# Performance work log

Measured on AMD Instinct MI355X. Metric: run time of the kernel, lower is better.

The kernel has to match this reference:

```python
import jax, jax.numpy as jnp
import numpy as np

B, N, IN_F, OUT_F, H = 16, 1024, 256, 256, 4
D = OUT_F // H  # head_dim = 64
NEG_SLOPE = 0.2


def setup_inputs() -> dict:
    key = jax.random.key(0)
    k1, k2, k3 = jax.random.split(key, 3)
    h = jax.random.normal(k1, (B, N, IN_F), dtype=jnp.float32)
    mask = jnp.ones((B, N), dtype=jnp.int32)
    W = jax.random.normal(k2, (OUT_F, IN_F), dtype=jnp.float32) * (1.0 / np.sqrt(IN_F))
    a = jax.random.normal(k3, (2 * D, 1), dtype=jnp.float32) * 0.1
    return {"h": h, "mask": mask, "W": W, "a": a}


def reference(h, mask, W, a):
    # Wh = h @ W.T -> (B, N, OUT_F) -> (B, H, N, D)
    Wh = jnp.einsum('bnf,of->bno', h, W)
    Wh = Wh.reshape(h.shape[0], h.shape[1], H, D).transpose(0, 2, 1, 3)
    # Additive split: cat([Wh_i, Wh_j]) @ a == Wh_i @ a1 + Wh_j @ a2 (same math,
    # avoids the O(N^2 * 2D) concat tensor)
    a1 = a[:D, 0]  # (D,)
    a2 = a[D:, 0]  # (D,)
    s1 = jnp.einsum('bhnd,d->bhn', Wh, a1)  # score for node i
    s2 = jnp.einsum('bhnd,d->bhn', Wh, a2)  # score for node j
    e = s1[:, :, :, None] + s2[:, :, None, :]          # (B, H, N, N)
    e = jnp.where(e >= 0, e, NEG_SLOPE * e)            # LeakyReLU(0.2)
    node_mask = mask.astype(bool)                      # (B, N)
    mm = node_mask[:, None, :, None] & node_mask[:, None, None, :]  # (B,1,N,N)
    e = jnp.where(mm, e, -jnp.inf)
    attn = jax.nn.softmax(e, axis=-1)
    # dropout is identity in eval mode
    attn = jnp.where(mm, attn, 0.0)
    h_prime = jnp.einsum('bhij,bhjd->bhid', attn, Wh)  # (B, H, N, D)
    h_prime = h_prime.transpose(0, 2, 1, 3).reshape(h.shape[0], h.shape[1], OUT_F)
    return h_prime * mask.astype(h_prime.dtype)[:, :, None]
```

## Files before the change

### kernel.cpp

```cpp
#include <hip/hip_runtime.h>

typedef short short8 __attribute__((ext_vector_type(8)));
typedef float floatx4 __attribute__((ext_vector_type(4)));
typedef float floatx16 __attribute__((ext_vector_type(16)));
typedef unsigned int u32;

#define NEG_SLOPE 0.2f

__device__ __forceinline__ u32 pk_rtne(float a, float b) {
    u32 ua = __float_as_uint(a); ua += 0x7fffu + ((ua >> 16) & 1u);
    u32 ub = __float_as_uint(b); ub += 0x7fffu + ((ub >> 16) & 1u);
    return __builtin_amdgcn_perm(ub, ua, 0x07060302);
}
__device__ __forceinline__ u32 pk_trunc(float a, float b) {
    return __builtin_amdgcn_perm(__float_as_uint(b), __float_as_uint(a), 0x07060302);
}
__device__ __forceinline__ void gl_lds16(const void* g, void* l) {
    __builtin_amdgcn_global_load_lds((__attribute__((address_space(1))) u32*)(void*)g,
                                     (__attribute__((address_space(3))) u32*)l, 16, 0, 0);
}

__global__ __launch_bounds__(256, 4) void k_prep(
    const float* __restrict__ W, const float* __restrict__ a,
    unsigned short* __restrict__ WFg, float* __restrict__ V1g,
    float* __restrict__ V2g)
{
    __shared__ float sV1[256], sV2[256];
    const int t = threadIdx.x;
    const int hh = blockIdx.x;
    const int lane = t & 63;

    sV1[t] = 0.f;
    sV2[t] = 0.f;
    __syncthreads();

    float vp1[8] = {0, 0, 0, 0, 0, 0, 0, 0};
    float vp2[8] = {0, 0, 0, 0, 0, 0, 0, 0};
    const int c = t & 31;
    const int rb = t >> 5;
#pragma unroll
    for (int i = 0; i < 8; ++i) {
        int row = i * 8 + rb;
        const float* gp = &W[((size_t)(hh * 64 + row)) * 256 + c * 8];
        float4 w0 = *(const float4*)gp;
        float4 w1 = *(const float4*)(gp + 4);
        float a1r = a[row], a2r = a[64 + row];
        vp1[0] += a1r * w0.x; vp1[1] += a1r * w0.y; vp1[2] += a1r * w0.z; vp1[3] += a1r * w0.w;
        vp1[4] += a1r * w1.x; vp1[5] += a1r * w1.y; vp1[6] += a1r * w1.z; vp1[7] += a1r * w1.w;
        vp2[0] += a2r * w0.x; vp2[1] += a2r * w0.y; vp2[2] += a2r * w0.z; vp2[3] += a2r * w0.w;
        vp2[4] += a2r * w1.x; vp2[5] += a2r * w1.y; vp2[6] += a2r * w1.z; vp2[7] += a2r * w1.w;
        uint4 pv;
        pv.x = pk_rtne(w0.x, w0.y); pv.y = pk_rtne(w0.z, w0.w);
        pv.z = pk_rtne(w1.x, w1.y); pv.w = pk_rtne(w1.z, w1.w);
        int kt = c >> 2, qq = c & 3, nt = row >> 4, r15 = row & 15;
        int idx16 = (kt * 4 + nt) * 64 + qq * 16 + r15;
        *(uint4*)&WFg[((size_t)hh * 2048 + idx16) * 8] = pv;
    }
#pragma unroll
    for (int j = 0; j < 8; ++j) {
        vp1[j] += __shfl_xor(vp1[j], 32, 64);
        vp2[j] += __shfl_xor(vp2[j], 32, 64);
    }
    if (lane < 32) {
#pragma unroll
        for (int j = 0; j < 8; ++j) {
            atomicAdd(&sV1[c * 8 + j], vp1[j]);
            atomicAdd(&sV2[c * 8 + j], vp2[j]);
        }
    }
    __syncthreads();
    V1g[hh * 256 + t] = sV1[t];
    V2g[hh * 256 + t] = sV2[t];
}

__global__ __launch_bounds__(256, 4) void k_wh(
    const float* __restrict__ hin, const int* __restrict__ mask,
    const unsigned short* __restrict__ WFg, const float* __restrict__ V1g,
    const float* __restrict__ V2g,
    unsigned short* __restrict__ WhF, float2* __restrict__ E1F1,
    float2* __restrict__ E2F2)
{
    __shared__ unsigned short sBF[8 * 4 * 64 * 8];
    __shared__ float sV1[256], sV2[256];

    const int t = threadIdx.x;
    const int bi = blockIdx.x;
    const int mtile = bi & 255, hh = bi >> 8;
    const int m0g = mtile * 64;
    const int b = m0g >> 10, i0 = m0g & 1023;
    const int b4h = b * 4 + hh;
    const int wid = t >> 6, lane = t & 63;
    const int l15 = lane & 15, q = lane >> 4;

    {
        const char* wsrc = (const char*)WFg + (size_t)hh * 32768;
#pragma unroll
        for (int r = 0; r < 8; ++r)
            gl_lds16(wsrc + r * 4096 + t * 16, (char*)sBF + r * 4096 + t * 16);
        if (wid == 0)
            gl_lds16((const char*)(V1g + hh * 256) + lane * 16, (char*)sV1 + lane * 16);
        if (wid == 1)
            gl_lds16((const char*)(V2g + hh * 256) + lane * 16, (char*)sV2 + lane * 16);
    }
    __syncthreads();

    floatx4 acc[4];
#pragma unroll
    for (int nt = 0; nt < 4; ++nt) {
        floatx4 z = {0.f, 0.f, 0.f, 0.f};
        acc[nt] = z;
    }
    float s1a = 0.f, s2a = 0.f;
    const float* hrow = &hin[((size_t)(m0g + wid * 16 + l15)) * 256 + q * 8];
#pragma unroll
    for (int kt = 0; kt < 8; ++kt) {
        float4 h0 = *(const float4*)(hrow + kt * 32);
        float4 h1 = *(const float4*)(hrow + kt * 32 + 4);
        float4 v1a = *(const float4*)&sV1[kt * 32 + q * 8];
        float4 v1b = *(const float4*)&sV1[kt * 32 + q * 8 + 4];
        float4 v2a = *(const float4*)&sV2[kt * 32 + q * 8];
        float4 v2b = *(const float4*)&sV2[kt * 32 + q * 8 + 4];
        s1a += h0.x * v1a.x + h0.y * v1a.y + h0.z * v1a.z + h0.w * v1a.w
             + h1.x * v1b.x + h1.y * v1b.y + h1.z * v1b.z + h1.w * v1b.w;
        s2a += h0.x * v2a.x + h0.y * v2a.y + h0.z * v2a.z + h0.w * v2a.w
             + h1.x * v2b.x + h1.y * v2b.y + h1.z * v2b.z + h1.w * v2b.w;
        union { short8 s; uint4 u; } af;
        af.u.x = pk_rtne(h0.x, h0.y); af.u.y = pk_rtne(h0.z, h0.w);
        af.u.z = pk_rtne(h1.x, h1.y); af.u.w = pk_rtne(h1.z, h1.w);
#pragma unroll
        for (int nt = 0; nt < 4; ++nt) {
            short8 bf = *(const short8*)&sBF[((kt * 4 + nt) * 64 + lane) * 8];
            acc[nt] = __builtin_amdgcn_mfma_f32_16x16x32_bf16(af.s, bf, acc[nt], 0, 0, 0);
        }
    }

    const int jt16 = (i0 >> 4) + wid;
    const int g = q & 1, jb = (q >> 1) * 4;
#pragma unroll
    for (int nt = 0; nt < 4; ++nt) {
        int nt32 = nt >> 1;
        int l31 = (nt & 1) * 16 + l15;
        uint2 pv;
        pv.x = pk_rtne(acc[nt][0], acc[nt][1]);
        pv.y = pk_rtne(acc[nt][2], acc[nt][3]);
        size_t idx = ((((size_t)b4h * 64 + jt16) * 2 + nt32) * 64 + (g * 32 + l31)) * 8 + jb;
        *(uint2*)&WhF[idx] = pv;
    }

    s1a += __shfl_xor(s1a, 16, 64); s1a += __shfl_xor(s1a, 32, 64);
    s2a += __shfl_xor(s2a, 16, 64); s2a += __shfl_xor(s2a, 32, 64);
    if (lane < 16) {
        int i = i0 + wid * 16 + lane;
        E1F1[(size_t)b4h * 1024 + i] = make_float2(__expf(s1a), __expf(NEG_SLOPE * s1a));
        int mj = mask[b * 1024 + i];
        E2F2[(size_t)b4h * 1024 + i] =
            make_float2(mj ? __expf(s2a) : 0.f, mj ? __expf(NEG_SLOPE * s2a) : 0.f);
    }
}

__global__ __launch_bounds__(256, 4) void k_attn(
    const int* __restrict__ mask,
    const unsigned short* __restrict__ WhF,
    const float2* __restrict__ E1F1, const float2* __restrict__ E2F2,
    float* __restrict__ out)
{
    __shared__ float2 sEF[1024];
    __shared__ float sRed[2][64][49];

    const int t = threadIdx.x;
    const int bi = blockIdx.x;
    const int b4h = bi & 63, ib = bi >> 6;
    const int b = b4h >> 2, hh = b4h & 3;
    const int i0 = ib * 64;
    const int wid = t >> 6, lane = t & 63;
    const int l31 = lane & 31, g = lane >> 5;
    const int rg = wid & 1, jh = wid >> 1;
    const int iw = i0 + rg * 32;

    {
        const char* src = (const char*)(E2F2 + (size_t)b4h * 1024);
        gl_lds16(src + t * 16, (char*)sEF + t * 16);
        gl_lds16(src + 4096 + t * 16, (char*)sEF + 4096 + t * 16);
    }

    float2 e1 = E1F1[(size_t)b4h * 1024 + iw + l31];
    const float E1 = e1.x, F1 = e1.y;

    floatx16 acc0, acc1, accL;
#pragma unroll
    for (int r = 0; r < 16; ++r) { acc0[r] = 0.f; acc1[r] = 0.f; accL[r] = 0.f; }
    const short ob = (short)0x3F80;
    const short8 ones = {ob, ob, ob, ob, ob, ob, ob, ob};

    const char* gbase = (const char*)WhF + (size_t)b4h * 131072 + (size_t)lane * 16;
    const int cb = jh * 32;

    short8 ga0 = *(const short8*)(gbase + (size_t)cb * 2048);
    short8 ga1 = *(const short8*)(gbase + (size_t)cb * 2048 + 1024);
    short8 gb0 = *(const short8*)(gbase + (size_t)(cb + 1) * 2048);
    short8 gb1 = *(const short8*)(gbase + (size_t)(cb + 1) * 2048 + 1024);

    __syncthreads();

    float4 nA0, nA1, nB0, nB1;
    {
        const float4* pA = (const float4*)&sEF[cb * 16 + g * 4];
        const float4* pB = (const float4*)&sEF[cb * 16 + 8 + g * 4];
        nA0 = pA[0]; nA1 = pA[1]; nB0 = pB[0]; nB1 = pB[1];
    }

#pragma unroll 4
    for (int cr = 0; cr < 32; cr += 2) {
        {
            const float4 eA0 = nA0, eA1 = nA1, eB0 = nB0, eB1 = nB1;
            const int cn = cb + ((cr + 1) & 31);
            const float4* pA = (const float4*)&sEF[cn * 16 + g * 4];
            const float4* pB = (const float4*)&sEF[cn * 16 + 8 + g * 4];
            nA0 = pA[0]; nA1 = pA[1]; nB0 = pB[0]; nB1 = pB[1];
            const short8 bf0 = ga0, bf1 = ga1;
            const int cg = cb + ((cr + 2) & 31);
            ga0 = *(const short8*)(gbase + (size_t)cg * 2048);
            ga1 = *(const short8*)(gbase + (size_t)cg * 2048 + 1024);
            float w0 = fmaxf(E1 * eA0.x, F1 * eA0.y);
            float w1 = fmaxf(E1 * eA0.z, F1 * eA0.w);
            float w2 = fmaxf(E1 * eA1.x, F1 * eA1.y);
            float w3 = fmaxf(E1 * eA1.z, F1 * eA1.w);
            float w4 = fmaxf(E1 * eB0.x, F1 * eB0.y);
            float w5 = fmaxf(E1 * eB0.z, F1 * eB0.w);
            float w6 = fmaxf(E1 * eB1.x, F1 * eB1.y);
            float w7 = fmaxf(E1 * eB1.z, F1 * eB1.w);
            union { short8 s; u32 u[4]; } af;
            af.u[0] = pk_trunc(w0, w1);
            af.u[1] = pk_trunc(w2, w3);
            af.u[2] = pk_trunc(w4, w5);
            af.u[3] = pk_trunc(w6, w7);
            acc0 = __builtin_amdgcn_mfma_f32_32x32x16_bf16(af.s, bf0, acc0, 0, 0, 0);
            acc1 = __builtin_amdgcn_mfma_f32_32x32x16_bf16(af.s, bf1, acc1, 0, 0, 0);
            accL = __builtin_amdgcn_mfma_f32_32x32x16_bf16(af.s, ones, accL, 0, 0, 0);
        }
        {
            const float4 eA0 = nA0, eA1 = nA1, eB0 = nB0, eB1 = nB1;
            const int cn = cb + ((cr + 2) & 31);
            const float4* pA = (const float4*)&sEF[cn * 16 + g * 4];
            const float4* pB = (const float4*)&sEF[cn * 16 + 8 + g * 4];
            nA0 = pA[0]; nA1 = pA[1]; nB0 = pB[0]; nB1 = pB[1];
            const short8 bf0 = gb0, bf1 = gb1;
            const int cg = cb + ((cr + 3) & 31);
            gb0 = *(const short8*)(gbase + (size_t)cg * 2048);
            gb1 = *(const short8*)(gbase + (size_t)cg * 2048 + 1024);
            float w0 = fmaxf(E1 * eA0.x, F1 * eA0.y);
            float w1 = fmaxf(E1 * eA0.z, F1 * eA0.w);
            float w2 = fmaxf(E1 * eA1.x, F1 * eA1.y);
            float w3 = fmaxf(E1 * eA1.z, F1 * eA1.w);
            float w4 = fmaxf(E1 * eB0.x, F1 * eB0.y);
            float w5 = fmaxf(E1 * eB0.z, F1 * eB0.w);
            float w6 = fmaxf(E1 * eB1.x, F1 * eB1.y);
            float w7 = fmaxf(E1 * eB1.z, F1 * eB1.w);
            union { short8 s; u32 u[4]; } af;
            af.u[0] = pk_trunc(w0, w1);
            af.u[1] = pk_trunc(w2, w3);
            af.u[2] = pk_trunc(w4, w5);
            af.u[3] = pk_trunc(w6, w7);
            acc0 = __builtin_amdgcn_mfma_f32_32x32x16_bf16(af.s, bf0, acc0, 0, 0, 0);
            acc1 = __builtin_amdgcn_mfma_f32_32x32x16_bf16(af.s, bf1, acc1, 0, 0, 0);
            accL = __builtin_amdgcn_mfma_f32_32x32x16_bf16(af.s, ones, accL, 0, 0, 0);
        }
    }

    if (jh == 1) {
        float* d = &sRed[rg][lane][0];
#pragma unroll
        for (int r = 0; r < 16; ++r) {
            d[r] = acc0[r]; d[16 + r] = acc1[r]; d[32 + r] = accL[r];
        }
    }
    __syncthreads();
    if (jh == 0) {
        const float* d = &sRed[rg][lane][0];
#pragma unroll
        for (int r = 0; r < 16; ++r) {
            acc0[r] += d[r]; acc1[r] += d[16 + r]; accL[r] += d[32 + r];
        }
#pragma unroll
        for (int r = 0; r < 16; ++r) {
            int row = (r & 3) + 8 * (r >> 2) + 4 * g;
            int i = iw + row;
            float l = accL[r];
            int mi = mask[b * 1024 + i];
            float inv = (mi && l > 0.f) ? 1.0f / l : 0.f;
            size_t o = ((size_t)(b * 1024 + i)) * 256 + hh * 64;
            out[o + l31] = acc0[r] * inv;
            out[o + 32 + l31] = acc1[r] * inv;
        }
    }
}

extern "C" void kernel_launch(void* const* d_in, const int* in_sizes, int n_in,
                              void* d_out, int out_size, void* d_ws, size_t ws_size,
                              hipStream_t stream) {
    const float* h = (const float*)d_in[0];
    const int* mask = (const int*)d_in[1];
    const float* W = (const float*)d_in[2];
    const float* a = (const float*)d_in[3];
    float* out = (float*)d_out;

    unsigned short* WhF = (unsigned short*)d_ws;
    float2* E1F1 = (float2*)((char*)d_ws + (size_t)8 * 1024 * 1024);
    float2* E2F2 = E1F1 + 64 * 1024;
    unsigned short* WFg = (unsigned short*)((char*)d_ws + (size_t)9 * 1024 * 1024);
    float* V1g = (float*)((char*)WFg + 4 * 16384 * sizeof(unsigned short));
    float* V2g = V1g + 1024;

    hipLaunchKernelGGL(k_prep, dim3(4), dim3(256), 0, stream, W, a, WFg, V1g, V2g);
    hipLaunchKernelGGL(k_wh, dim3(1024), dim3(256), 0, stream, h, mask, WFg, V1g, V2g, WhF, E1F1, E2F2);
    hipLaunchKernelGGL(k_attn, dim3(1024), dim3(256), 0, stream, mask, WhF, E1F1, E2F2, out);
}
```

Measured before the change: 101.7 us.

## Prepermute E2F2 exponent table and read it from global instead of LDS

k_wh now writes the per-node exp scores in a permuted layout, so each lane's eight needed values for one MFMA k-step are contiguous. k_attn then loads them directly from global memory (cached in L1/L2) as four float4s, dropping the LDS staging buffer, the global-to-LDS copy and the block barrier. This lowers LDS use and removes a sync, but the inner loop now issues extra global loads that may add latency.

```diff
diff --git a/kernel.cpp b/kernel.cpp
--- a/kernel.cpp
+++ b/kernel.cpp
@@ -78,7 +78,7 @@
     const unsigned short* __restrict__ WFg, const float* __restrict__ V1g,
     const float* __restrict__ V2g,
     unsigned short* __restrict__ WhF, float2* __restrict__ E1F1,
-    float2* __restrict__ E2F2)
+    float2* __restrict__ EFp)
 {
     __shared__ unsigned short sBF[8 * 4 * 64 * 8];
     __shared__ float sV1[256], sV2[256];
@@ -153,18 +153,20 @@
         int i = i0 + wid * 16 + lane;
         E1F1[(size_t)b4h * 1024 + i] = make_float2(__expf(s1a), __expf(NEG_SLOPE * s1a));
         int mj = mask[b * 1024 + i];
-        E2F2[(size_t)b4h * 1024 + i] =
-            make_float2(mj ? __expf(s2a) : 0.f, mj ? __expf(NEG_SLOPE * s2a) : 0.f);
+        float e2v = mj ? __expf(s2a) : 0.f;
+        float f2v = mj ? __expf(NEG_SLOPE * s2a) : 0.f;
+        int cc = i >> 4, rr = i & 15;
+        int gg = (rr >> 2) & 1, jj = (rr & 3) + 4 * (rr >> 3);
+        EFp[(size_t)b4h * 1024 + (cc * 2 + gg) * 8 + jj] = make_float2(e2v, f2v);
     }
 }
 
 __global__ __launch_bounds__(256, 4) void k_attn(
     const int* __restrict__ mask,
     const unsigned short* __restrict__ WhF,
-    const float2* __restrict__ E1F1, const float2* __restrict__ E2F2,
+    const float2* __restrict__ E1F1, const float2* __restrict__ EFp,
     float* __restrict__ out)
 {
-    __shared__ float2 sEF[1024];
     __shared__ float sRed[2][64][49];
 
     const int t = threadIdx.x;
@@ -177,12 +179,6 @@
     const int rg = wid & 1, jh = wid >> 1;
     const int iw = i0 + rg * 32;
 
-    {
-        const char* src = (const char*)(E2F2 + (size_t)b4h * 1024);
-        gl_lds16(src + t * 16, (char*)sEF + t * 16);
-        gl_lds16(src + 4096 + t * 16, (char*)sEF + 4096 + t * 16);
-    }
-
     float2 e1 = E1F1[(size_t)b4h * 1024 + iw + l31];
     const float E1 = e1.x, F1 = e1.y;
 
@@ -193,42 +189,38 @@
     const short8 ones = {ob, ob, ob, ob, ob, ob, ob, ob};
 
     const char* gbase = (const char*)WhF + (size_t)b4h * 131072 + (size_t)lane * 16;
+    const float4* efb = (const float4*)(EFp + (size_t)b4h * 1024);
     const int cb = jh * 32;
 
     short8 ga0 = *(const short8*)(gbase + (size_t)cb * 2048);
     short8 ga1 = *(const short8*)(gbase + (size_t)cb * 2048 + 1024);
     short8 gb0 = *(const short8*)(gbase + (size_t)(cb + 1) * 2048);
     short8 gb1 = *(const short8*)(gbase + (size_t)(cb + 1) * 2048 + 1024);
-
-    __syncthreads();
-
-    float4 nA0, nA1, nB0, nB1;
+    float4 nE0, nE1, nE2, nE3;
     {
-        const float4* pA = (const float4*)&sEF[cb * 16 + g * 4];
-        const float4* pB = (const float4*)&sEF[cb * 16 + 8 + g * 4];
-        nA0 = pA[0]; nA1 = pA[1]; nB0 = pB[0]; nB1 = pB[1];
+        const float4* p = efb + (size_t)(cb * 2 + g) * 4;
+        nE0 = p[0]; nE1 = p[1]; nE2 = p[2]; nE3 = p[3];
     }
 
 #pragma unroll 4
     for (int cr = 0; cr < 32; cr += 2) {
         {
-            const float4 eA0 = nA0, eA1 = nA1, eB0 = nB0, eB1 = nB1;
+            const float4 e0 = nE0, e1v = nE1, e2v = nE2, e3v = nE3;
             const int cn = cb + ((cr + 1) & 31);
-            const float4* pA = (const float4*)&sEF[cn * 16 + g * 4];
-            const float4* pB = (const float4*)&sEF[cn * 16 + 8 + g * 4];
-            nA0 = pA[0]; nA1 = pA[1]; nB0 = pB[0]; nB1 = pB[1];
+            const float4* p = efb + (size_t)(cn * 2 + g) * 4;
+            nE0 = p[0]; nE1 = p[1]; nE2 = p[2]; nE3 = p[3];
             const short8 bf0 = ga0, bf1 = ga1;
             const int cg = cb + ((cr + 2) & 31);
             ga0 = *(const short8*)(gbase + (size_t)cg * 2048);
             ga1 = *(const short8*)(gbase + (size_t)cg * 2048 + 1024);
-            float w0 = fmaxf(E1 * eA0.x, F1 * eA0.y);
-            float w1 = fmaxf(E1 * eA0.z, F1 * eA0.w);
-            float w2 = fmaxf(E1 * eA1.x, F1 * eA1.y);
-            float w3 = fmaxf(E1 * eA1.z, F1 * eA1.w);
-            float w4 = fmaxf(E1 * eB0.x, F1 * eB0.y);
-            float w5 = fmaxf(E1 * eB0.z, F1 * eB0.w);
-            float w6 = fmaxf(E1 * eB1.x, F1 * eB1.y);
-            float w7 = fmaxf(E1 * eB1.z, F1 * eB1.w);
+            float w0 = fmaxf(E1 * e0.x, F1 * e0.y);
+            float w1 = fmaxf(E1 * e0.z, F1 * e0.w);
+            float w2 = fmaxf(E1 * e1v.x, F1 * e1v.y);
+            float w3 = fmaxf(E1 * e1v.z, F1 * e1v.w);
+            float w4 = fmaxf(E1 * e2v.x, F1 * e2v.y);
+            float w5 = fmaxf(E1 * e2v.z, F1 * e2v.w);
+            float w6 = fmaxf(E1 * e3v.x, F1 * e3v.y);
+            float w7 = fmaxf(E1 * e3v.z, F1 * e3v.w);
             union { short8 s; u32 u[4]; } af;
             af.u[0] = pk_trunc(w0, w1);
             af.u[1] = pk_trunc(w2, w3);
@@ -239,23 +231,22 @@
             accL = __builtin_amdgcn_mfma_f32_32x32x16_bf16(af.s, ones, accL, 0, 0, 0);
         }
         {
-            const float4 eA0 = nA0, eA1 = nA1, eB0 = nB0, eB1 = nB1;
+            const float4 e0 = nE0, e1v = nE1, e2v = nE2, e3v = nE3;
             const int cn = cb + ((cr + 2) & 31);
-            const float4* pA = (const float4*)&sEF[cn * 16 + g * 4];
-            const float4* pB = (const float4*)&sEF[cn * 16 + 8 + g * 4];
-            nA0 = pA[0]; nA1 = pA[1]; nB0 = pB[0]; nB1 = pB[1];
+            const float4* p = efb + (size_t)(cn * 2 + g) * 4;
+            nE0 = p[0]; nE1 = p[1]; nE2 = p[2]; nE3 = p[3];
             const short8 bf0 = gb0, bf1 = gb1;
             const int cg = cb + ((cr + 3) & 31);
             gb0 = *(const short8*)(gbase + (size_t)cg * 2048);
             gb1 = *(const short8*)(gbase + (size_t)cg * 2048 + 1024);
-            float w0 = fmaxf(E1 * eA0.x, F1 * eA0.y);
-            float w1 = fmaxf(E1 * eA0.z, F1 * eA0.w);
-            float w2 = fmaxf(E1 * eA1.x, F1 * eA1.y);
-            float w3 = fmaxf(E1 * eA1.z, F1 * eA1.w);
-            float w4 = fmaxf(E1 * eB0.x, F1 * eB0.y);
-            float w5 = fmaxf(E1 * eB0.z, F1 * eB0.w);
-            float w6 = fmaxf(E1 * eB1.x, F1 * eB1.y);
-            float w7 = fmaxf(E1 * eB1.z, F1 * eB1.w);
+            float w0 = fmaxf(E1 * e0.x, F1 * e0.y);
+            float w1 = fmaxf(E1 * e0.z, F1 * e0.w);
+            float w2 = fmaxf(E1 * e1v.x, F1 * e1v.y);
+            float w3 = fmaxf(E1 * e1v.z, F1 * e1v.w);
+            float w4 = fmaxf(E1 * e2v.x, F1 * e2v.y);
+            float w5 = fmaxf(E1 * e2v.z, F1 * e2v.w);
+            float w6 = fmaxf(E1 * e3v.x, F1 * e3v.y);
+            float w7 = fmaxf(E1 * e3v.z, F1 * e3v.w);
             union { short8 s; u32 u[4]; } af;
             af.u[0] = pk_trunc(w0, w1);
             af.u[1] = pk_trunc(w2, w3);
@@ -306,12 +297,12 @@
 
     unsigned short* WhF = (unsigned short*)d_ws;
     float2* E1F1 = (float2*)((char*)d_ws + (size_t)8 * 1024 * 1024);
-    float2* E2F2 = E1F1 + 64 * 1024;
+    float2* EFp = E1F1 + 64 * 1024;
     unsigned short* WFg = (unsigned short*)((char*)d_ws + (size_t)9 * 1024 * 1024);
     float* V1g = (float*)((char*)WFg + 4 * 16384 * sizeof(unsigned short));
     float* V2g = V1g + 1024;
 
     hipLaunchKernelGGL(k_prep, dim3(4), dim3(256), 0, stream, W, a, WFg, V1g, V2g);
-    hipLaunchKernelGGL(k_wh, dim3(1024), dim3(256), 0, stream, h, mask, WFg, V1g, V2g, WhF, E1F1, E2F2);
-    hipLaunchKernelGGL(k_attn, dim3(1024), dim3(256), 0, stream, mask, WhF, E1F1, E2F2, out);
-}
+    hipLaunchKernelGGL(k_wh, dim3(1024), dim3(256), 0, stream, h, mask, WFg, V1g, V2g, WhF, E1F1, EFp);
+    hipLaunchKernelGGL(k_attn, dim3(1024), dim3(256), 0, stream, mask, WhF, E1F1, EFp, out);
+}
```

Result: slower. 125.0 us (+22.8%).
